# Kernel tuning notes

Measured on AMD Instinct MI355X. Metric: run time of the kernel, lower is better.

The kernel has to match this reference:

```python
import jax, jax.numpy as jnp
import numpy as np

N_NODES = 50000
N_EDGES = 600000
F_IN = 128
HID = 128
N_CLASSES = 10


def _gcn_graph(edge_index, n_nodes):
    # PyG GCNConv: add self-loops, deg computed on target (col) with weight 1,
    # norm_e = deg^-1/2[src] * deg^-1/2[dst]
    src = jnp.concatenate([edge_index[0], jnp.arange(n_nodes, dtype=edge_index.dtype)])
    dst = jnp.concatenate([edge_index[1], jnp.arange(n_nodes, dtype=edge_index.dtype)])
    deg = jax.ops.segment_sum(jnp.ones_like(dst, dtype=jnp.float32), dst, num_segments=n_nodes)
    dinv = jnp.where(deg > 0, jax.lax.rsqrt(deg), 0.0)
    norm = dinv[src] * dinv[dst]  # [E+N]
    return src, dst, norm


def _gcn_layer(x, W, b, src, dst, norm, n_nodes):
    h = x @ W                      # [N, out] linear first (bias applied post-agg)
    m = h[src] * norm[:, None]     # gather + scale, [E+N, out]
    out = jax.ops.segment_sum(m, dst, num_segments=n_nodes)  # scatter-add
    return out + b


def setup_inputs() -> dict:
    key = jax.random.key(0)
    ks = jax.random.split(key, 4)
    x = jax.random.normal(ks[0], (N_NODES, F_IN), dtype=jnp.float32)
    edge_index = jax.random.randint(ks[1], (2, N_EDGES), 0, N_NODES, dtype=jnp.int64)
    # Glorot-ish init scale for weights
    W_stack = jax.random.normal(ks[2], (8, HID, HID), dtype=jnp.float32) * (1.0 / np.sqrt(HID))
    b_stack = jnp.zeros((8, HID), dtype=jnp.float32)
    W_out = jax.random.normal(ks[3], (HID, N_CLASSES), dtype=jnp.float32) * (1.0 / np.sqrt(HID))
    b_out = jnp.zeros((N_CLASSES,), dtype=jnp.float32)
    return {"x": x, "edge_index": edge_index, "W_stack": W_stack, "b_stack": b_stack,
            "W_out": W_out, "b_out": b_out}


def reference(x, edge_index, W_stack, b_stack, W_out, b_out):
    n_nodes = x.shape[0]
    src, dst, norm = _gcn_graph(edge_index, n_nodes)
    h = x
    for i in range(8):  # conv1..conv8 with ELU
        h = jax.nn.elu(_gcn_layer(h, W_stack[i], b_stack[i], src, dst, norm, n_nodes))
    # conv9: no activation
    return _gcn_layer(h, W_out, b_out, src, dst, norm, n_nodes)
```

## Files before the change

kernel.cpp:

```cpp
#include <hip/hip_runtime.h>
#include <math.h>

#define NN 50000
#define NE 600000
#define HID 128
#define NCLS 10
#define T2S 16

typedef __bf16 bf16x8 __attribute__((ext_vector_type(8)));
typedef float f32x16 __attribute__((ext_vector_type(16)));

__device__ __forceinline__ void split3(float f, ushort& h, ushort& m, ushort& l) {
    unsigned uh = __float_as_uint(f) & 0xffff0000u;
    float fm = f - __uint_as_float(uh);
    unsigned um = __float_as_uint(fm) & 0xffff0000u;
    float fl = fm - __uint_as_float(um);
    h = (ushort)(uh >> 16);
    m = (ushort)(um >> 16);
    l = (ushort)(__float_as_uint(fl) >> 16);
}


__global__ __launch_bounds__(256) void k_count(const int* __restrict__ edge,
                                               int* __restrict__ counts) {
    int e = blockIdx.x * 256 + threadIdx.x;
    if (e < NE) atomicAdd(&counts[edge[NE + e]], 1);
}

__device__ __forceinline__ int wave_incl_scan(int x, int lane) {
#pragma unroll
    for (int off = 1; off < 64; off <<= 1) {
        int y = __shfl_up(x, off, 64);
        if (lane >= off) x += y;
    }
    return x;
}

__global__ __launch_bounds__(256) void k_scan1(const int* __restrict__ counts,
                                               int* __restrict__ rowptr,
                                               int* __restrict__ bsum,
                                               float* __restrict__ dinv) {
    __shared__ int ws[4];
    int tid = threadIdx.x;
    int i = blockIdx.x * 256 + tid;
    int lane = tid & 63, wv = tid >> 6;
    int v = (i < NN) ? counts[i] : 0;
    if (i < NN) dinv[i] = rsqrtf((float)(v + 1));
    int x = wave_incl_scan(v, lane);
    if (lane == 63) ws[wv] = x;
    __syncthreads();
    int off = 0;
    for (int j = 0; j < wv; ++j) off += ws[j];
    if (i < NN) rowptr[i] = off + x - v;
    if (tid == 255) bsum[blockIdx.x] = off + x;
}

__global__ __launch_bounds__(256) void k_scan2(int* __restrict__ bsum, int n) {
    __shared__ int ws[4];
    int tid = threadIdx.x;
    int lane = tid & 63, wv = tid >> 6;
    int v = (tid < n) ? bsum[tid] : 0;
    int x = wave_incl_scan(v, lane);
    if (lane == 63) ws[wv] = x;
    __syncthreads();
    int off = 0;
    for (int j = 0; j < wv; ++j) off += ws[j];
    __syncthreads();
    if (tid < n) bsum[tid] = off + x - v;
}

__global__ __launch_bounds__(256) void k_scan3(int* __restrict__ rowptr,
                                               const int* __restrict__ bsum) {
    int i = blockIdx.x * 256 + threadIdx.x;
    if (i < NN) rowptr[i] += bsum[blockIdx.x];
    if (i == 0) rowptr[NN] = NE;
}

__global__ __launch_bounds__(256) void k_fill(const int* __restrict__ edge,
                                              const int* __restrict__ rowptr,
                                              int* __restrict__ cursor,
                                              const float* __restrict__ dinv,
                                              int2* __restrict__ csr) {
    int e = blockIdx.x * 256 + threadIdx.x;
    if (e >= NE) return;
    int s = edge[e], d = edge[NE + e];
    int slot = atomicSub(&cursor[d], 1) - 1;
    csr[rowptr[d] + slot] = make_int2(s, __float_as_int(dinv[s] * dinv[d]));
}


__global__ __launch_bounds__(256) void k_split_w(const float* __restrict__ Wst,
                                                 ushort* __restrict__ Wt4) {
    int i = blockIdx.x * 256 + threadIdx.x;
    if (i >= 8 * HID * HID) return;
    int l = i >> 14;
    int k = (i >> 7) & 127;
    int n = i & 127;
    ushort h, m, lo;
    split3(Wst[i], h, m, lo);
    int ks = k >> 4, r = k & 15;
    size_t base = ((((size_t)l * 3) * 8 + ks) * 128 + n) * 16 + r;
    const size_t pstride = (size_t)8 * 128 * 16;
    Wt4[base] = h;
    Wt4[base + pstride] = m;
    Wt4[base + 2 * pstride] = lo;
}


__global__ __launch_bounds__(256) void k_mfma_gemm(const float* __restrict__ H,
                                                   const ushort* __restrict__ Wt,
                                                   float* __restrict__ T) {
    int tid = threadIdx.x;
    int lane = tid & 63, w = tid >> 6;
    int l31 = lane & 31, lh = lane >> 5;
    int rowbase = blockIdx.x * 128;

    int grow = rowbase + w * 32 + l31;
    if (grow >= NN) grow = NN - 1;
    const float* arow = H + (size_t)grow * HID + lh * 8;
    const ushort* wbase = Wt + (size_t)l31 * 16 + lh * 8;

    f32x16 acc[4] = {};

#pragma unroll 2
    for (int s = 0; s < 8; ++s) {
        const float4* ap = (const float4*)(arow + s * 16);
        float4 f0 = ap[0], f1 = ap[1];
        float av[8] = {f0.x, f0.y, f0.z, f0.w, f1.x, f1.y, f1.z, f1.w};
        union { ushort u[8]; bf16x8 v; } ah, am, al;
#pragma unroll
        for (int q = 0; q < 8; ++q) split3(av[q], ah.u[q], am.u[q], al.u[q]);

        uint4 bf[3][4];
#pragma unroll
        for (int p = 0; p < 3; ++p)
#pragma unroll
            for (int c = 0; c < 4; ++c)
                bf[p][c] = *(const uint4*)(wbase + (((size_t)p * 8 + s) * 128 + c * 32) * 16);

#pragma unroll
        for (int c = 0; c < 4; ++c)
            acc[c] = __builtin_amdgcn_mfma_f32_32x32x16_bf16(ah.v, *(const bf16x8*)&bf[0][c], acc[c], 0, 0, 0);
#pragma unroll
        for (int c = 0; c < 4; ++c)
            acc[c] = __builtin_amdgcn_mfma_f32_32x32x16_bf16(ah.v, *(const bf16x8*)&bf[1][c], acc[c], 0, 0, 0);
#pragma unroll
        for (int c = 0; c < 4; ++c)
            acc[c] = __builtin_amdgcn_mfma_f32_32x32x16_bf16(am.v, *(const bf16x8*)&bf[0][c], acc[c], 0, 0, 0);
#pragma unroll
        for (int c = 0; c < 4; ++c)
            acc[c] = __builtin_amdgcn_mfma_f32_32x32x16_bf16(ah.v, *(const bf16x8*)&bf[2][c], acc[c], 0, 0, 0);
#pragma unroll
        for (int c = 0; c < 4; ++c)
            acc[c] = __builtin_amdgcn_mfma_f32_32x32x16_bf16(am.v, *(const bf16x8*)&bf[1][c], acc[c], 0, 0, 0);
#pragma unroll
        for (int c = 0; c < 4; ++c)
            acc[c] = __builtin_amdgcn_mfma_f32_32x32x16_bf16(al.v, *(const bf16x8*)&bf[0][c], acc[c], 0, 0, 0);
    }

#pragma unroll
    for (int c = 0; c < 4; ++c)
#pragma unroll
        for (int reg = 0; reg < 16; ++reg) {
            int r = (reg & 3) + 8 * (reg >> 2) + 4 * lh;
            int gr = rowbase + w * 32 + r;
            if (gr < NN)
                T[(size_t)gr * HID + c * 32 + l31] = acc[c][reg];
        }
}

__device__ __forceinline__ void gather_to_lds(const float* __restrict__ Tin,
                                              const int* __restrict__ rowptr,
                                              const int2* __restrict__ csr,
                                              const float* __restrict__ dinv,
                                              float4 bv, float* Hs,
                                              int rowbase, int w, int slot, int l31,
                                              int nodes_per_wave) {
    for (int i = 0; i < nodes_per_wave; ++i) {
        int lrow = w * nodes_per_wave + i;
        int node = rowbase + lrow;
        if (node >= NN) node = NN - 1;
        int beg = rowptr[node], end = rowptr[node + 1];
        float sn = dinv[node];

        float4 acc = {0.f, 0.f, 0.f, 0.f};
        if (slot == 1) {
            float4 tv = ((const float4*)(Tin + (size_t)node * HID))[l31];
            float s2 = sn * sn;
            acc.x = s2 * tv.x + bv.x;
            acc.y = s2 * tv.y + bv.y;
            acc.z = s2 * tv.z + bv.z;
            acc.w = s2 * tv.w + bv.w;
        }

        const int2 zed = make_int2(0, 0);
        int p = beg + slot;
        int2 e0 = (p < end) ? csr[p] : zed;
        int2 e1 = (p + 2 < end) ? csr[p + 2] : zed;
        int2 e2 = (p + 4 < end) ? csr[p + 4] : zed;
        int2 e3 = (p + 6 < end) ? csr[p + 6] : zed;
        for (; p < end; p += 8) {
            float4 u0 = ((const float4*)(Tin + (size_t)e0.x * HID))[l31];
            float4 u1 = ((const float4*)(Tin + (size_t)e1.x * HID))[l31];
            float4 u2 = ((const float4*)(Tin + (size_t)e2.x * HID))[l31];
            float4 u3 = ((const float4*)(Tin + (size_t)e3.x * HID))[l31];
            float w0 = __int_as_float(e0.y), w1 = __int_as_float(e1.y);
            float w2 = __int_as_float(e2.y), w3 = __int_as_float(e3.y);
            e0 = (p + 8 < end) ? csr[p + 8] : zed;
            e1 = (p + 10 < end) ? csr[p + 10] : zed;
            e2 = (p + 12 < end) ? csr[p + 12] : zed;
            e3 = (p + 14 < end) ? csr[p + 14] : zed;
            acc.x += w0 * u0.x; acc.y += w0 * u0.y; acc.z += w0 * u0.z; acc.w += w0 * u0.w;
            acc.x += w1 * u1.x; acc.y += w1 * u1.y; acc.z += w1 * u1.z; acc.w += w1 * u1.w;
            acc.x += w2 * u2.x; acc.y += w2 * u2.y; acc.z += w2 * u2.z; acc.w += w2 * u2.w;
            acc.x += w3 * u3.x; acc.y += w3 * u3.y; acc.z += w3 * u3.z; acc.w += w3 * u3.w;
        }

        acc.x += __shfl_xor(acc.x, 32, 64);
        acc.y += __shfl_xor(acc.y, 32, 64);
        acc.z += __shfl_xor(acc.z, 32, 64);
        acc.w += __shfl_xor(acc.w, 32, 64);

        if (slot == 0) {
            float4 r = acc;
            r.x = r.x > 0.f ? r.x : expm1f(r.x);
            r.y = r.y > 0.f ? r.y : expm1f(r.y);
            r.z = r.z > 0.f ? r.z : expm1f(r.z);
            r.w = r.w > 0.f ? r.w : expm1f(r.w);
            int byte = lrow * 512 + l31 * 16;
            byte ^= (lrow & 7) << 4;
            *(float4*)((char*)Hs + byte) = r;
        }
    }
}


__global__ __launch_bounds__(512) void k_fused(const float* __restrict__ Tin,
                                               const ushort* __restrict__ Wt,
                                               const int* __restrict__ rowptr,
                                               const int2* __restrict__ csr,
                                               const float* __restrict__ dinv,
                                               const float* __restrict__ bias,
                                               float* __restrict__ Tout) {
    __shared__ float Hs[64 * 128];
    int tid = threadIdx.x;
    int lane = tid & 63, w = tid >> 6;
    int slot = lane >> 5, l31 = lane & 31;
    int rowbase = blockIdx.x * 64;

    float4 bv = ((const float4*)bias)[l31];

    gather_to_lds(Tin, rowptr, csr, dinv, bv, Hs, rowbase, w, slot, l31, 8);
    __syncthreads();

    int lh = slot;
    int rloc = (w >> 2) * 32 + l31;
    int colb = w & 3;
    const ushort* wbase = Wt + ((size_t)(colb * 32) + l31) * 16 + lh * 8;

    f32x16 acc2 = {};

#pragma unroll 2
    for (int s = 0; s < 8; ++s) {
        int byte = rloc * 512 + s * 64 + lh * 32;
        int sw = (rloc & 7) << 4;
        float4 f0 = *(const float4*)((const char*)Hs + (byte ^ sw));
        float4 f1 = *(const float4*)((const char*)Hs + ((byte + 16) ^ sw));
        float av[8] = {f0.x, f0.y, f0.z, f0.w, f1.x, f1.y, f1.z, f1.w};
        union { ushort u[8]; bf16x8 v; } ah, am, al;
#pragma unroll
        for (int q = 0; q < 8; ++q) split3(av[q], ah.u[q], am.u[q], al.u[q]);

        uint4 bf[3];
#pragma unroll
        for (int p = 0; p < 3; ++p)
            bf[p] = *(const uint4*)(wbase + (((size_t)p * 8 + s) * 128) * 16);

        acc2 = __builtin_amdgcn_mfma_f32_32x32x16_bf16(ah.v, *(const bf16x8*)&bf[0], acc2, 0, 0, 0);
        acc2 = __builtin_amdgcn_mfma_f32_32x32x16_bf16(ah.v, *(const bf16x8*)&bf[1], acc2, 0, 0, 0);
        acc2 = __builtin_amdgcn_mfma_f32_32x32x16_bf16(am.v, *(const bf16x8*)&bf[0], acc2, 0, 0, 0);
        acc2 = __builtin_amdgcn_mfma_f32_32x32x16_bf16(ah.v, *(const bf16x8*)&bf[2], acc2, 0, 0, 0);
        acc2 = __builtin_amdgcn_mfma_f32_32x32x16_bf16(am.v, *(const bf16x8*)&bf[1], acc2, 0, 0, 0);
        acc2 = __builtin_amdgcn_mfma_f32_32x32x16_bf16(al.v, *(const bf16x8*)&bf[0], acc2, 0, 0, 0);
    }

#pragma unroll
    for (int reg = 0; reg < 16; ++reg) {
        int r = (reg & 3) + 8 * (reg >> 2) + 4 * lh;
        int gr = rowbase + (w >> 2) * 32 + r;
        if (gr < NN)
            Tout[(size_t)gr * HID + colb * 32 + l31] = acc2[reg];
    }
}


__global__ __launch_bounds__(512) void k_fused_out(const float* __restrict__ Tin,
                                                   const float* __restrict__ W,
                                                   const int* __restrict__ rowptr,
                                                   const int2* __restrict__ csr,
                                                   const float* __restrict__ dinv,
                                                   const float* __restrict__ bias,
                                                   float* __restrict__ T2) {
    __shared__ float Hs[64 * 128];
    __shared__ float Ws[128 * 11];
    int tid = threadIdx.x;
    int lane = tid & 63, w = tid >> 6;
    int slot = lane >> 5, l31 = lane & 31;
    int rowbase = blockIdx.x * 64;

    for (int m = tid; m < HID * NCLS; m += 512) {
        int k = m / NCLS, c = m - k * NCLS;
        Ws[k * 11 + c] = W[m];
    }

    float4 bv = ((const float4*)bias)[l31];
    gather_to_lds(Tin, rowptr, csr, dinv, bv, Hs, rowbase, w, slot, l31, 8);
    __syncthreads();

    int row = tid >> 3;
    int t8 = tid & 7;
    float acc[NCLS];
#pragma unroll
    for (int c = 0; c < NCLS; ++c) acc[c] = 0.f;
    int sw = (row & 7) << 4;
    int base = row * 512 + t8 * 64;
#pragma unroll
    for (int q = 0; q < 4; ++q) {
        float4 f = *(const float4*)((const char*)Hs + ((base + q * 16) ^ sw));
        float hv[4] = {f.x, f.y, f.z, f.w};
#pragma unroll
        for (int j = 0; j < 4; ++j) {
            const float* wr = &Ws[(t8 * 16 + q * 4 + j) * 11];
#pragma unroll
            for (int c = 0; c < NCLS; ++c) acc[c] += hv[j] * wr[c];
        }
    }
#pragma unroll
    for (int off = 4; off >= 1; off >>= 1) {
#pragma unroll
        for (int c = 0; c < NCLS; ++c) acc[c] += __shfl_xor(acc[c], off, 8);
    }
    int gr = rowbase + row;
    if (t8 == 0 && gr < NN) {
#pragma unroll
        for (int c = 0; c < NCLS; ++c) T2[(size_t)gr * T2S + c] = acc[c];
    }
}

__global__ __launch_bounds__(256) void k_gather_out(const float* __restrict__ T2,
                                                    float* __restrict__ out,
                                                    const int* __restrict__ rowptr,
                                                    const int2* __restrict__ csr,
                                                    const float* __restrict__ dinv,
                                                    const float* __restrict__ bias) {
    int lane = threadIdx.x & 63;
    int node = (blockIdx.x * 256 + threadIdx.x) >> 6;
    if (node >= NN) return;
    int slot = lane >> 4, c = lane & 15;
    int beg = rowptr[node], end = rowptr[node + 1];
    float acc = 0.f;
    if (c < NCLS) {
        for (int i = beg + slot; i < end; i += 4) {
            int2 e = csr[i];
            acc += __int_as_float(e.y) * T2[(size_t)e.x * T2S + c];
        }
    }
    acc += __shfl_xor(acc, 16, 64);
    acc += __shfl_xor(acc, 32, 64);
    if (slot == 0 && c < NCLS) {
        float sn = dinv[node];
        sn *= sn;
        out[node * NCLS + c] = acc + sn * T2[(size_t)node * T2S + c] + bias[c];
    }
}


extern "C" void kernel_launch(void* const* d_in, const int* in_sizes, int n_in,
                              void* d_out, int out_size, void* d_ws, size_t ws_size,
                              hipStream_t stream) {
    (void)in_sizes; (void)n_in; (void)out_size; (void)ws_size;
    const float* x       = (const float*)d_in[0];
    const int*   edge    = (const int*)d_in[1];
    const float* W_stack = (const float*)d_in[2];
    const float* b_stack = (const float*)d_in[3];
    const float* W_out   = (const float*)d_in[4];
    const float* b_out   = (const float*)d_in[5];
    float* out = (float*)d_out;

    char* ws = (char*)d_ws;
    const size_t bigbuf = (size_t)NN * HID * sizeof(float);
    float* X      = (float*)ws;
    float* Y      = (float*)(ws + bigbuf);
    char*  p      = ws + 2 * bigbuf;
    int2*  csr    = (int2*)p;              p += sizeof(int2) * NE;
    float* dinv   = (float*)p;             p += sizeof(float) * NN;
    int*   rowptr = (int*)p;               p += sizeof(int) * (NN + 1);
    int*   counts = (int*)p;               p += sizeof(int) * NN;
    int*   bsum   = (int*)p;               p += sizeof(int) * 256;
    p = (char*)(((size_t)p + 15) & ~(size_t)15);
    ushort* Wt4 = (ushort*)p;  p += sizeof(ushort) * 8 * 3 * HID * HID;
    float* T2b  = (float*)p;   p += sizeof(float) * NN * T2S;

    const int NB_N  = (NN + 255) / 256;
    const int NB_E  = (NE + 255) / 256;
    const int NB_G  = (NN + 127) / 128;
    const int NB_F  = (NN + 63) / 64;
    const int NB_A  = (NN * 64 + 255) / 256;
    const int NB_SW = (8 * HID * HID + 255) / 256;

    hipMemsetAsync(counts, 0, sizeof(int) * NN, stream);
    k_count<<<NB_E, 256, 0, stream>>>(edge, counts);
    k_scan1<<<NB_N, 256, 0, stream>>>(counts, rowptr, bsum, dinv);
    k_scan2<<<1, 256, 0, stream>>>(bsum, NB_N);
    k_scan3<<<NB_N, 256, 0, stream>>>(rowptr, bsum);
    k_fill<<<NB_E, 256, 0, stream>>>(edge, rowptr, counts, dinv, csr);

    k_split_w<<<NB_SW, 256, 0, stream>>>(W_stack, Wt4);

    k_mfma_gemm<<<NB_G, 256, 0, stream>>>(x, Wt4, Y);

    float* cur = Y;
    float* nxt = X;
    for (int l = 0; l < 7; ++l) {
        k_fused<<<NB_F, 512, 0, stream>>>(cur, Wt4 + (size_t)(l + 1) * 3 * HID * HID,
                                          rowptr, csr, dinv,
                                          b_stack + (size_t)l * HID, nxt);
        float* t = cur; cur = nxt; nxt = t;
    }

    k_fused_out<<<NB_F, 512, 0, stream>>>(cur, W_out, rowptr, csr, dinv,
                                          b_stack + (size_t)7 * HID, T2b);

    k_gather_out<<<NB_A, 256, 0, stream>>>(T2b, out, rowptr, csr, dinv, b_out);
}
```

Baseline: 733.2 us.

## Halve fused-layer block to 32 rows with two MFMA waves per block

The fused gather+GEMM kernels now process 32 rows per 256-thread block instead of 64 rows per 512-thread block, which halves LDS use per block. In the GEMM phase only two waves do work, and each computes two 32x32 output tiles, so each split A fragment is reused across 64 columns. The aim is to fit more resident blocks per CU, hide gather latency better, and cut the redundant split3 work per wave. The cost is that half the waves sit idle during the MFMA phase and the grid has twice as many blocks.

Measured after the change: 693.8 us. -5.4%, faster.

```diff
diff --git a/kernel.cpp b/kernel.cpp
--- a/kernel.cpp
+++ b/kernel.cpp
@@ -235,35 +235,36 @@
 }
 
 
-__global__ __launch_bounds__(512) void k_fused(const float* __restrict__ Tin,
+__global__ __launch_bounds__(256) void k_fused(const float* __restrict__ Tin,
                                                const ushort* __restrict__ Wt,
                                                const int* __restrict__ rowptr,
                                                const int2* __restrict__ csr,
                                                const float* __restrict__ dinv,
                                                const float* __restrict__ bias,
                                                float* __restrict__ Tout) {
-    __shared__ float Hs[64 * 128];
+    __shared__ float Hs[32 * 128];
     int tid = threadIdx.x;
     int lane = tid & 63, w = tid >> 6;
     int slot = lane >> 5, l31 = lane & 31;
-    int rowbase = blockIdx.x * 64;
+    int rowbase = blockIdx.x * 32;
 
     float4 bv = ((const float4*)bias)[l31];
 
     gather_to_lds(Tin, rowptr, csr, dinv, bv, Hs, rowbase, w, slot, l31, 8);
     __syncthreads();
 
+    if (w >= 2) return;
+
     int lh = slot;
-    int rloc = (w >> 2) * 32 + l31;
-    int colb = w & 3;
-    const ushort* wbase = Wt + ((size_t)(colb * 32) + l31) * 16 + lh * 8;
-
-    f32x16 acc2 = {};
+    int colh = w;
+    const ushort* wbase = Wt + ((size_t)(colh * 64) + l31) * 16 + lh * 8;
+
+    f32x16 acc2[2] = {};
 
 #pragma unroll 2
     for (int s = 0; s < 8; ++s) {
-        int byte = rloc * 512 + s * 64 + lh * 32;
-        int sw = (rloc & 7) << 4;
+        int byte = l31 * 512 + s * 64 + lh * 32;
+        int sw = (l31 & 7) << 4;
         float4 f0 = *(const float4*)((const char*)Hs + (byte ^ sw));
         float4 f1 = *(const float4*)((const char*)Hs + ((byte + 16) ^ sw));
         float av[8] = {f0.x, f0.y, f0.z, f0.w, f1.x, f1.y, f1.z, f1.w};
@@ -271,44 +272,60 @@
 #pragma unroll
         for (int q = 0; q < 8; ++q) split3(av[q], ah.u[q], am.u[q], al.u[q]);
 
-        uint4 bf[3];
+        uint4 bf[3][2];
 #pragma unroll
         for (int p = 0; p < 3; ++p)
-            bf[p] = *(const uint4*)(wbase + (((size_t)p * 8 + s) * 128) * 16);
-
-        acc2 = __builtin_amdgcn_mfma_f32_32x32x16_bf16(ah.v, *(const bf16x8*)&bf[0], acc2, 0, 0, 0);
-        acc2 = __builtin_amdgcn_mfma_f32_32x32x16_bf16(ah.v, *(const bf16x8*)&bf[1], acc2, 0, 0, 0);
-        acc2 = __builtin_amdgcn_mfma_f32_32x32x16_bf16(am.v, *(const bf16x8*)&bf[0], acc2, 0, 0, 0);
-        acc2 = __builtin_amdgcn_mfma_f32_32x32x16_bf16(ah.v, *(const bf16x8*)&bf[2], acc2, 0, 0, 0);
-        acc2 = __builtin_amdgcn_mfma_f32_32x32x16_bf16(am.v, *(const bf16x8*)&bf[1], acc2, 0, 0, 0);
-        acc2 = __builtin_amdgcn_mfma_f32_32x32x16_bf16(al.v, *(const bf16x8*)&bf[0], acc2, 0, 0, 0);
-    }
-
-#pragma unroll
-    for (int reg = 0; reg < 16; ++reg) {
-        int r = (reg & 3) + 8 * (reg >> 2) + 4 * lh;
-        int gr = rowbase + (w >> 2) * 32 + r;
-        if (gr < NN)
-            Tout[(size_t)gr * HID + colb * 32 + l31] = acc2[reg];
-    }
-}
-
-
-__global__ __launch_bounds__(512) void k_fused_out(const float* __restrict__ Tin,
+#pragma unroll
+            for (int c = 0; c < 2; ++c)
+                bf[p][c] = *(const uint4*)(wbase + (((size_t)p * 8 + s) * 128 + c * 32) * 16);
+
+#pragma unroll
+        for (int c = 0; c < 2; ++c)
+            acc2[c] = __builtin_amdgcn_mfma_f32_32x32x16_bf16(ah.v, *(const bf16x8*)&bf[0][c], acc2[c], 0, 0, 0);
+#pragma unroll
+        for (int c = 0; c < 2; ++c)
+            acc2[c] = __builtin_amdgcn_mfma_f32_32x32x16_bf16(ah.v, *(const bf16x8*)&bf[1][c], acc2[c], 0, 0, 0);
+#pragma unroll
+        for (int c = 0; c < 2; ++c)
+            acc2[c] = __builtin_amdgcn_mfma_f32_32x32x16_bf16(am.v, *(const bf16x8*)&bf[0][c], acc2[c], 0, 0, 0);
+#pragma unroll
+        for (int c = 0; c < 2; ++c)
+            acc2[c] = __builtin_amdgcn_mfma_f32_32x32x16_bf16(ah.v, *(const bf16x8*)&bf[2][c], acc2[c], 0, 0, 0);
+#pragma unroll
+        for (int c = 0; c < 2; ++c)
+            acc2[c] = __builtin_amdgcn_mfma_f32_32x32x16_bf16(am.v, *(const bf16x8*)&bf[1][c], acc2[c], 0, 0, 0);
+#pragma unroll
+        for (int c = 0; c < 2; ++c)
+            acc2[c] = __builtin_amdgcn_mfma_f32_32x32x16_bf16(al.v, *(const bf16x8*)&bf[0][c], acc2[c], 0, 0, 0);
+    }
+
+#pragma unroll
+    for (int c = 0; c < 2; ++c)
+#pragma unroll
+        for (int reg = 0; reg < 16; ++reg) {
+            int r = (reg & 3) + 8 * (reg >> 2) + 4 * lh;
+            int gr = rowbase + r;
+            if (gr < NN)
+                Tout[(size_t)gr * HID + colh * 64 + c * 32 + l31] = acc2[c][reg];
+        }
+}
+
+
+__global__ __launch_bounds__(256) void k_fused_out(const float* __restrict__ Tin,
                                                    const float* __restrict__ W,
                                                    const int* __restrict__ rowptr,
                                                    const int2* __restrict__ csr,
                                                    const float* __restrict__ dinv,
                                                    const float* __restrict__ bias,
                                                    float* __restrict__ T2) {
-    __shared__ float Hs[64 * 128];
+    __shared__ float Hs[32 * 128];
     __shared__ float Ws[128 * 11];
     int tid = threadIdx.x;
     int lane = tid & 63, w = tid >> 6;
     int slot = lane >> 5, l31 = lane & 31;
-    int rowbase = blockIdx.x * 64;
-
-    for (int m = tid; m < HID * NCLS; m += 512) {
+    int rowbase = blockIdx.x * 32;
+
+    for (int m = tid; m < HID * NCLS; m += 256) {
         int k = m / NCLS, c = m - k * NCLS;
         Ws[k * 11 + c] = W[m];
     }
@@ -404,7 +421,7 @@
     const int NB_N  = (NN + 255) / 256;
     const int NB_E  = (NE + 255) / 256;
     const int NB_G  = (NN + 127) / 128;
-    const int NB_F  = (NN + 63) / 64;
+    const int NB_F  = (NN + 31) / 32;
     const int NB_A  = (NN * 64 + 255) / 256;
     const int NB_SW = (8 * HID * HID + 255) / 256;
 
@@ -422,13 +439,13 @@
     float* cur = Y;
     float* nxt = X;
     for (int l = 0; l < 7; ++l) {
-        k_fused<<<NB_F, 512, 0, stream>>>(cur, Wt4 + (size_t)(l + 1) * 3 * HID * HID,
+        k_fused<<<NB_F, 256, 0, stream>>>(cur, Wt4 + (size_t)(l + 1) * 3 * HID * HID,
                                           rowptr, csr, dinv,
                                           b_stack + (size_t)l * HID, nxt);
         float* t = cur; cur = nxt; nxt = t;
     }
 
-    k_fused_out<<<NB_F, 512, 0, stream>>>(cur, W_out, rowptr, csr, dinv,
+    k_fused_out<<<NB_F, 256, 0, stream>>>(cur, W_out, rowptr, csr, dinv,
                                           b_stack + (size_t)7 * HID, T2b);
 
     k_gather_out<<<NB_A, 256, 0, stream>>>(T2b, out, rowptr, csr, dinv, b_out);
```
